# Optimization experiments

Hardware: AMD Instinct MI355X
Metric: run time of the kernel (lower is better)

Reference implementation:

```python
import math
import jax, jax.numpy as jnp
import numpy as np

C, H, R, PD = 256, 6, 32, 16
HEAD_SCALE = 1.0 / math.sqrt(R)


def setup_inputs() -> dict:
    key = jax.random.key(0)
    ks = jax.random.split(key, 8)
    B, Lp1 = 8, 4097
    feats = jax.random.normal(ks[0], (B, Lp1, C), dtype=jnp.float32)
    # params (stored [in, out] for x @ W)
    Wq = jax.random.normal(ks[1], (C, H * R), dtype=jnp.float32) / math.sqrt(C)
    Wk = jax.random.normal(ks[2], (C, H * R), dtype=jnp.float32) / math.sqrt(C)
    Wpi = jax.random.normal(ks[3], (C, PD), dtype=jnp.float32) / math.sqrt(C)
    bpi = jnp.zeros((PD,), jnp.float32)
    Wpj = jax.random.normal(ks[4], (C, PD), dtype=jnp.float32) / math.sqrt(C)
    bpj = jnp.zeros((PD,), jnp.float32)
    Wd = jax.random.normal(ks[5], (C, 1), dtype=jnp.float32) / math.sqrt(C)
    bd = jnp.zeros((1,), jnp.float32)
    alpha_pair = jnp.float32(0.5)
    logit_scale = jnp.float32(1.0)
    return {"feats": feats, "Wq": Wq, "Wk": Wk, "Wpi": Wpi, "bpi": bpi,
            "Wpj": Wpj, "bpj": bpj, "Wd": Wd, "bd": bd,
            "alpha_pair": alpha_pair, "logit_scale": logit_scale}


def _fold_vertices(feats):
    x = feats[:, 1:]                      # drop first token
    B, L, Cc = x.shape
    return x.reshape(B, L // 2, 2, Cc).mean(axis=2)  # [B, N, C]


def reference(feats, Wq, Wk, Wpi, bpi, Wpj, bpj, Wd, bd, alpha_pair, logit_scale):
    x = _fold_vertices(feats)             # [B, N, C]
    B, N, _ = x.shape
    Q = (x @ Wq).reshape(B, N, H, R)
    K = (x @ Wk).reshape(B, N, H, R)
    # sum over heads fused into one contraction (math-equal to per-head scores summed)
    S = jnp.einsum('bnhr,bmhr->bnm', Q, K) * HEAD_SCALE   # [B, N, N]
    a_i = jax.nn.relu(x @ Wpi + bpi)      # [B, N, PD]
    b_j = jax.nn.relu(x @ Wpj + bpj)
    S = S + jnp.maximum(alpha_pair, 0.0) * jnp.einsum('bnd,bmd->bnm', a_i, b_j)
    d = (x @ Wd + bd)[..., 0]             # [B, N]
    idx = jnp.arange(N)
    S = S.at[:, idx, idx].add(d)
    return S * jnp.maximum(logit_scale, 0.01)
```

## Files before the change

### kernel.cpp

```cpp
#include <hip/hip_runtime.h>
#include <hip/hip_bf16.h>
#include <stdint.h>

typedef __attribute__((ext_vector_type(8))) short short8;
typedef __attribute__((ext_vector_type(4))) short short4v;
typedef __attribute__((ext_vector_type(4))) float f32x4;
typedef __attribute__((ext_vector_type(4))) unsigned uint4v;

#define NB 8
#define NN 2048
#define CC 256
#define LP1 4097
#define HR 192
#define PDim 16
#define KP 224
#define NPAD 448
#define HEAD_SCALE 0.17677669529663689f

#define GLOAD16(g, l) __builtin_amdgcn_global_load_lds( \
    (const __attribute__((address_space(1))) unsigned int*)(g), \
    (__attribute__((address_space(3))) unsigned int*)(l), 16, 0, 0)

static __device__ __forceinline__ unsigned short bf16bits(float f) {
    __hip_bfloat16 h = __float2bfloat16(f);
    return *(unsigned short*)&h;
}

__global__ __launch_bounds__(256) void k0_prep(
    const float* __restrict__ Wq, const float* __restrict__ Wk,
    const float* __restrict__ Wpi, const float* __restrict__ Wpj,
    const float* __restrict__ Wd,
    __hip_bfloat16* __restrict__ WT,
    unsigned* __restrict__ Ppad, unsigned* __restrict__ Rpad)
{
    const int WTN = NPAD*CC;
    const int PV  = NB*NN*2;
    int i = blockIdx.x*blockDim.x + threadIdx.x;
    if (i < WTN) {
        int c = i >> 8, k = i & 255;
        float v;
        if (c < HR)                 v = Wq[k*HR + c] * HEAD_SCALE;
        else if (c < 2*HR)          v = Wk[k*HR + (c-HR)];
        else if (c < 2*HR+PDim)     v = Wpi[k*PDim + (c-2*HR)];
        else if (c < 2*HR+2*PDim)   v = Wpj[k*PDim + (c-2*HR-PDim)];
        else if (c == 416)          v = Wd[k];
        else                        v = 0.f;
        WT[i] = __float2bfloat16(v);
    } else {
        int j = i - WTN;
        unsigned* arr = (j < PV) ? Ppad : Rpad;
        int q = (j < PV) ? j : j - PV;
        int row = q >> 1, of = 104 + (q & 1)*4;
        *(uint4v*)(arr + (size_t)row*(KP/2) + of) = (uint4v){0,0,0,0};
    }
}

__global__ __launch_bounds__(256, 3) void ka_proj(
    const float* __restrict__ feats, const __hip_bfloat16* __restrict__ WT,
    const float* __restrict__ bpi, const float* __restrict__ bpj,
    const float* __restrict__ bd, const float* __restrict__ alpha_pair,
    __hip_bfloat16* __restrict__ P, __hip_bfloat16* __restrict__ R,
    float* __restrict__ dvec)
{
    __shared__ __hip_bfloat16 ldsA[32*256];
    __shared__ __hip_bfloat16 ldsB[448*32];

    int t = threadIdx.x;
    int lane = t & 63;
    int w = t >> 6;
    int l15 = lane & 15, lg = lane >> 4;
    int hw = blockIdx.x;
    int b = hw & 7;
    int n0loc = (hw >> 3) * 32;

    int scol = (((t & 3) ^ ((t >> 4) & 3)) << 4);
    const char* srcB[7];
    int wofB[7];
#pragma unroll
    for (int i = 0; i < 7; ++i) {
        int row = i*64 + (t >> 2);
        srcB[i] = (const char*)WT + (size_t)row*512 + scol;
        wofB[i] = row*64 + ((t & 3) << 4);
    }

    uint4v st[7];
#pragma unroll
    for (int i = 0; i < 7; ++i) st[i] = *(const uint4v*)(srcB[i]);

    {
        int r = t >> 3, cg = t & 7;
        size_t fb = ((size_t)b*LP1 + 1 + 2*(size_t)(n0loc + r))*CC + cg*32;
#pragma unroll
        for (int s = 0; s < 4; ++s) {
            float4 a0 = *(const float4*)(feats + fb + s*8);
            float4 a1 = *(const float4*)(feats + fb + s*8 + 4);
            float4 c0 = *(const float4*)(feats + fb + CC + s*8);
            float4 c1 = *(const float4*)(feats + fb + CC + s*8 + 4);
            unsigned short h[8];
            h[0] = bf16bits(0.5f*(a0.x + c0.x));
            h[1] = bf16bits(0.5f*(a0.y + c0.y));
            h[2] = bf16bits(0.5f*(a0.z + c0.z));
            h[3] = bf16bits(0.5f*(a0.w + c0.w));
            h[4] = bf16bits(0.5f*(a1.x + c1.x));
            h[5] = bf16bits(0.5f*(a1.y + c1.y));
            h[6] = bf16bits(0.5f*(a1.z + c1.z));
            h[7] = bf16bits(0.5f*(a1.w + c1.w));
            int slot = (cg*4 + s) ^ (r & 7);
            *(short8*)((char*)ldsA + r*512 + slot*16) = *(const short8*)h;
        }
    }

#pragma unroll
    for (int i = 0; i < 7; ++i)
        *(uint4v*)((char*)ldsB + wofB[i]) = st[i];
    __syncthreads();

    f32x4 acc[7][2];
#pragma unroll
    for (int ni = 0; ni < 7; ++ni)
#pragma unroll
        for (int mi = 0; mi < 2; ++mi)
            acc[ni][mi] = (f32x4){0.f, 0.f, 0.f, 0.f};

    int arow[2];
#pragma unroll
    for (int mi = 0; mi < 2; ++mi) arow[mi] = (mi*16 + l15)*512;
    int rx = l15 & 7;
    int bbase = (w*112 + l15)*64 + ((lg ^ ((l15 >> 2) & 3)) << 4);

#pragma unroll
    for (int kk = 0; kk < 8; ++kk) {
        if (kk < 7) {
#pragma unroll
            for (int i = 0; i < 7; ++i)
                st[i] = *(const uint4v*)(srcB[i] + (size_t)(kk + 1)*64);
        }
        short8 a[2], bb[7];
        int slotb = ((kk*4 + lg) ^ rx) << 4;
#pragma unroll
        for (int mi = 0; mi < 2; ++mi)
            a[mi] = *(const short8*)((const char*)ldsA + arow[mi] + slotb);
#pragma unroll
        for (int ni = 0; ni < 7; ++ni)
            bb[ni] = *(const short8*)((const char*)ldsB + bbase + ni*1024);
#pragma unroll
        for (int ni = 0; ni < 7; ++ni)
#pragma unroll
            for (int mi = 0; mi < 2; ++mi)
                acc[ni][mi] = __builtin_amdgcn_mfma_f32_16x16x32_bf16(
                    bb[ni], a[mi], acc[ni][mi], 0, 0, 0);

        __syncthreads();
        if (kk < 7) {
#pragma unroll
            for (int i = 0; i < 7; ++i)
                *(uint4v*)((char*)ldsB + wofB[i]) = st[i];
            __syncthreads();
        }
    }

    float alpha_eff = fmaxf(alpha_pair[0], 0.f);
    float bd0 = bd[0];
#pragma unroll
    for (int ni = 0; ni < 7; ++ni) {
        int cb = w*112 + ni*16 + lg*4;
#pragma unroll
        for (int mi = 0; mi < 2; ++mi) {
            int n = n0loc + mi*16 + l15;
            size_t rb = ((size_t)b*NN + n)*KP;
            f32x4 v = acc[ni][mi];
            if (cb < HR) {
                short4v h;
#pragma unroll
                for (int j = 0; j < 4; ++j) h[j] = (short)bf16bits(v[j]);
                *(short4v*)(P + rb + cb) = h;
            } else if (cb < 2*HR) {
                short4v h;
#pragma unroll
                for (int j = 0; j < 4; ++j) h[j] = (short)bf16bits(v[j]);
                *(short4v*)(R + rb + (cb - HR)) = h;
            } else if (cb < 2*HR + PDim) {
                int pc = cb - 2*HR;
                short4v h;
#pragma unroll
                for (int j = 0; j < 4; ++j)
                    h[j] = (short)bf16bits(fmaxf(v[j] + bpi[pc+j], 0.f) * alpha_eff);
                *(short4v*)(P + rb + HR + pc) = h;
            } else if (cb < 2*HR + 2*PDim) {
                int pc = cb - 2*HR - PDim;
                short4v h;
#pragma unroll
                for (int j = 0; j < 4; ++j)
                    h[j] = (short)bf16bits(fmaxf(v[j] + bpj[pc+j], 0.f));
                *(short4v*)(R + rb + HR + pc) = h;
            } else if (cb == 416) {
                dvec[(size_t)b*NN + n] = v[0] + bd0;
            }
        }
    }
}

__global__ __launch_bounds__(256, 4) void kb_pair(
    const __hip_bfloat16* __restrict__ P, const __hip_bfloat16* __restrict__ R,
    const float* __restrict__ dvec, const float* __restrict__ logit_scale,
    float* __restrict__ out)
{
    __shared__ __hip_bfloat16 ldsA[2][128*32];
    __shared__ __hip_bfloat16 ldsB[2][128*32];

    int t = threadIdx.x;
    int lane = t & 63;
    int w = t >> 6;
    int wr = w >> 1, wc = w & 1;
    int l15 = lane & 15, lg = lane >> 4;

    int hw = blockIdx.x;
    int b = hw & 7;
    int within = hw >> 3;
    int m0 = (within & 15) << 7;
    int n0 = (within >> 4) << 7;

    const char* srcA[2];
    const char* srcB[2];
    {
        int scolb = (((t & 3) ^ ((t >> 4) & 3)) << 4);
#pragma unroll
        for (int i = 0; i < 2; ++i) {
            int row = i*64 + (t >> 2);
            srcA[i] = (const char*)(P + ((size_t)b*NN + n0 + row)*KP) + scolb;
            srcB[i] = (const char*)(R + ((size_t)b*NN + m0 + row)*KP) + scolb;
        }
    }
    int ldst = w * 1024;

    int abyte = (wr*64 + l15)*64 + ((lg ^ ((l15 >> 2) & 3)) << 4);
    int bbyte = (wc*64 + l15)*64 + ((lg ^ ((l15 >> 2) & 3)) << 4);

    f32x4 acc[4][4];
#pragma unroll
    for (int ni = 0; ni < 4; ++ni)
#pragma unroll
        for (int mi = 0; mi < 4; ++mi)
            acc[ni][mi] = (f32x4){0.f, 0.f, 0.f, 0.f};

#pragma unroll
    for (int i = 0; i < 2; ++i) {
        GLOAD16(srcA[i], (char*)(&ldsA[0][0]) + i*4096 + ldst);
        GLOAD16(srcB[i], (char*)(&ldsB[0][0]) + i*4096 + ldst);
    }
#pragma unroll
    for (int i = 0; i < 2; ++i) {
        GLOAD16(srcA[i] + 64, (char*)(&ldsA[1][0]) + i*4096 + ldst);
        GLOAD16(srcB[i] + 64, (char*)(&ldsB[1][0]) + i*4096 + ldst);
    }

#pragma unroll
    for (int s = 0; s < 7; ++s) {
        if (s < 6) asm volatile("s_waitcnt vmcnt(4)" ::: "memory");
        else       asm volatile("s_waitcnt vmcnt(0)" ::: "memory");
        __builtin_amdgcn_s_barrier();
        __builtin_amdgcn_sched_barrier(0);

        const int buf = s & 1;
        short8 a[4], bb[4];
#pragma unroll
        for (int mi = 0; mi < 4; ++mi)
            a[mi] = *(const short8*)((const char*)(&ldsA[buf][0]) + abyte + mi*1024);
#pragma unroll
        for (int ni = 0; ni < 4; ++ni)
            bb[ni] = *(const short8*)((const char*)(&ldsB[buf][0]) + bbyte + ni*1024);
#pragma unroll
        for (int ni = 0; ni < 4; ++ni)
#pragma unroll
            for (int mi = 0; mi < 4; ++mi)
                acc[ni][mi] = __builtin_amdgcn_mfma_f32_16x16x32_bf16(
                    bb[ni], a[mi], acc[ni][mi], 0, 0, 0);

        __builtin_amdgcn_sched_barrier(0);
        __builtin_amdgcn_s_barrier();
        if (s + 2 < 7) {
            size_t kof = (size_t)(s + 2) * 64;
#pragma unroll
            for (int i = 0; i < 2; ++i) {
                GLOAD16(srcA[i] + kof, (char*)(&ldsA[buf][0]) + i*4096 + ldst);
                GLOAD16(srcB[i] + kof, (char*)(&ldsB[buf][0]) + i*4096 + ldst);
            }
        }
    }

    float ls = fmaxf(logit_scale[0], 0.01f);
    bool diag_tile = (n0 == m0);
#pragma unroll
    for (int mi = 0; mi < 4; ++mi) {
        int orow = n0 + wr*64 + mi*16 + l15;
        float* orow_p = out + ((size_t)b*NN + orow)*NN;
        float dval = diag_tile ? dvec[(size_t)b*NN + orow] : 0.f;
#pragma unroll
        for (int ni = 0; ni < 4; ++ni) {
            int cbase = m0 + wc*64 + ni*16 + lg*4;
            f32x4 v = acc[ni][mi];
            if (diag_tile) {
                int dj = orow - cbase;
                if (dj >= 0 && dj < 4) v[dj] += dval;
            }
            f32x4 o;
#pragma unroll
            for (int j = 0; j < 4; ++j) o[j] = v[j] * ls;
            *(f32x4*)(orow_p + cbase) = o;
        }
    }
}

extern "C" void kernel_launch(void* const* d_in, const int* in_sizes, int n_in,
                              void* d_out, int out_size, void* d_ws, size_t ws_size,
                              hipStream_t stream)
{
    const float* feats = (const float*)d_in[0];
    const float* Wq    = (const float*)d_in[1];
    const float* Wk    = (const float*)d_in[2];
    const float* Wpi   = (const float*)d_in[3];
    const float* bpi   = (const float*)d_in[4];
    const float* Wpj   = (const float*)d_in[5];
    const float* bpj   = (const float*)d_in[6];
    const float* Wd    = (const float*)d_in[7];
    const float* bd    = (const float*)d_in[8];
    const float* alpha = (const float*)d_in[9];
    const float* lsc   = (const float*)d_in[10];

    char* ws = (char*)d_ws;
    __hip_bfloat16* WT = (__hip_bfloat16*)(ws);
    __hip_bfloat16* P  = (__hip_bfloat16*)(ws + 229376);
    __hip_bfloat16* R  = (__hip_bfloat16*)(ws + 7569408);
    float*          dv = (float*)(ws + 14909440);

    k0_prep<<<704, 256, 0, stream>>>(Wq, Wk, Wpi, Wpj, Wd,
                                     WT, (unsigned*)P, (unsigned*)R);
    ka_proj<<<512, 256, 0, stream>>>(feats, WT, bpi, bpj, bd, alpha, P, R, dv);
    kb_pair<<<2048, 256, 0, stream>>>(P, R, dv, lsc, (float*)d_out);
}
```

Baseline: 63.96 us.

## Compute two adjacent column tiles per block with a continuous load pipeline

```diff
diff --git a/kernel.cpp b/kernel.cpp
--- a/kernel.cpp
+++ b/kernel.cpp
@@ -216,9 +216,10 @@
 
     int hw = blockIdx.x;
     int b = hw & 7;
-    int within = hw >> 3;
-    int m0 = (within & 15) << 7;
-    int n0 = (within >> 4) << 7;
+    int p = hw >> 3;
+    int n0 = (p >> 3) << 7;
+    int m0base = (p & 7) << 8;
+    const size_t TOFF = 128 * KP * 2;
 
     const char* srcA[2];
     const char* srcB[2];
@@ -228,7 +229,7 @@
         for (int i = 0; i < 2; ++i) {
             int row = i*64 + (t >> 2);
             srcA[i] = (const char*)(P + ((size_t)b*NN + n0 + row)*KP) + scolb;
-            srcB[i] = (const char*)(R + ((size_t)b*NN + m0 + row)*KP) + scolb;
+            srcB[i] = (const char*)(R + ((size_t)b*NN + m0base + row)*KP) + scolb;
         }
     }
     int ldst = w * 1024;
@@ -236,6 +237,8 @@
     int abyte = (wr*64 + l15)*64 + ((lg ^ ((l15 >> 2) & 3)) << 4);
     int bbyte = (wc*64 + l15)*64 + ((lg ^ ((l15 >> 2) & 3)) << 4);
 
+    float ls = fmaxf(logit_scale[0], 0.01f);
+
     f32x4 acc[4][4];
 #pragma unroll
     for (int ni = 0; ni < 4; ++ni)
@@ -243,24 +246,17 @@
         for (int mi = 0; mi < 4; ++mi)
             acc[ni][mi] = (f32x4){0.f, 0.f, 0.f, 0.f};
 
-#pragma unroll
-    for (int i = 0; i < 2; ++i) {
-        GLOAD16(srcA[i], (char*)(&ldsA[0][0]) + i*4096 + ldst);
-        GLOAD16(srcB[i], (char*)(&ldsB[0][0]) + i*4096 + ldst);
-    }
-#pragma unroll
-    for (int i = 0; i < 2; ++i) {
-        GLOAD16(srcA[i] + 64, (char*)(&ldsA[1][0]) + i*4096 + ldst);
-        GLOAD16(srcB[i] + 64, (char*)(&ldsB[1][0]) + i*4096 + ldst);
-    }
-
-#pragma unroll
-    for (int s = 0; s < 7; ++s) {
-        if (s < 6) asm volatile("s_waitcnt vmcnt(4)" ::: "memory");
-        else       asm volatile("s_waitcnt vmcnt(0)" ::: "memory");
-        __builtin_amdgcn_s_barrier();
-        __builtin_amdgcn_sched_barrier(0);
-
+    auto STAGE = [&](int step) {
+        size_t kof = (size_t)(step % 7) * 64;
+        size_t bof = (step >= 7) ? TOFF : 0;
+        int buf = step & 1;
+        GLOAD16(srcA[0] + kof,       (char*)(&ldsA[buf][0]) + 0*4096 + ldst);
+        GLOAD16(srcB[0] + bof + kof, (char*)(&ldsB[buf][0]) + 0*4096 + ldst);
+        GLOAD16(srcA[1] + kof,       (char*)(&ldsA[buf][0]) + 1*4096 + ldst);
+        GLOAD16(srcB[1] + bof + kof, (char*)(&ldsB[buf][0]) + 1*4096 + ldst);
+    };
+
+    auto COMPUTE = [&](int s) {
         const int buf = s & 1;
         short8 a[4], bb[4];
 #pragma unroll
@@ -275,40 +271,65 @@
             for (int mi = 0; mi < 4; ++mi)
                 acc[ni][mi] = __builtin_amdgcn_mfma_f32_16x16x32_bf16(
                     bb[ni], a[mi], acc[ni][mi], 0, 0, 0);
-
+    };
+
+    auto EPILOGUE = [&](int m0t) {
+        bool diag_tile = (n0 == m0t);
+#pragma unroll
+        for (int mi = 0; mi < 4; ++mi) {
+            int orow = n0 + wr*64 + mi*16 + l15;
+            float* orow_p = out + ((size_t)b*NN + orow)*NN;
+            float dval = diag_tile ? dvec[(size_t)b*NN + orow] : 0.f;
+#pragma unroll
+            for (int ni = 0; ni < 4; ++ni) {
+                int cbase = m0t + wc*64 + ni*16 + lg*4;
+                f32x4 v = acc[ni][mi];
+                if (diag_tile) {
+                    int dj = orow - cbase;
+                    if (dj >= 0 && dj < 4) v[dj] += dval;
+                }
+                f32x4 o;
+#pragma unroll
+                for (int j = 0; j < 4; ++j) o[j] = v[j] * ls;
+                *(f32x4*)(orow_p + cbase) = o;
+            }
+        }
+    };
+
+    STAGE(0);
+    STAGE(1);
+
+#pragma unroll
+    for (int s = 0; s < 7; ++s) {
+        asm volatile("s_waitcnt vmcnt(4)" ::: "memory");
+        __builtin_amdgcn_s_barrier();
+        __builtin_amdgcn_sched_barrier(0);
+        COMPUTE(s);
         __builtin_amdgcn_sched_barrier(0);
         __builtin_amdgcn_s_barrier();
-        if (s + 2 < 7) {
-            size_t kof = (size_t)(s + 2) * 64;
-#pragma unroll
-            for (int i = 0; i < 2; ++i) {
-                GLOAD16(srcA[i] + kof, (char*)(&ldsA[buf][0]) + i*4096 + ldst);
-                GLOAD16(srcB[i] + kof, (char*)(&ldsB[buf][0]) + i*4096 + ldst);
-            }
-        }
-    }
-
-    float ls = fmaxf(logit_scale[0], 0.01f);
-    bool diag_tile = (n0 == m0);
-#pragma unroll
-    for (int mi = 0; mi < 4; ++mi) {
-        int orow = n0 + wr*64 + mi*16 + l15;
-        float* orow_p = out + ((size_t)b*NN + orow)*NN;
-        float dval = diag_tile ? dvec[(size_t)b*NN + orow] : 0.f;
-#pragma unroll
-        for (int ni = 0; ni < 4; ++ni) {
-            int cbase = m0 + wc*64 + ni*16 + lg*4;
-            f32x4 v = acc[ni][mi];
-            if (diag_tile) {
-                int dj = orow - cbase;
-                if (dj >= 0 && dj < 4) v[dj] += dval;
-            }
-            f32x4 o;
-#pragma unroll
-            for (int j = 0; j < 4; ++j) o[j] = v[j] * ls;
-            *(f32x4*)(orow_p + cbase) = o;
-        }
-    }
+        STAGE(s + 2);
+    }
+
+    EPILOGUE(m0base);
+#pragma unroll
+    for (int ni = 0; ni < 4; ++ni)
+#pragma unroll
+        for (int mi = 0; mi < 4; ++mi)
+            acc[ni][mi] = (f32x4){0.f, 0.f, 0.f, 0.f};
+
+#pragma unroll
+    for (int s = 7; s < 14; ++s) {
+        if (s < 13) asm volatile("s_waitcnt vmcnt(4)" ::: "memory");
+        else        asm volatile("s_waitcnt vmcnt(0)" ::: "memory");
+        __builtin_amdgcn_s_barrier();
+        __builtin_amdgcn_sched_barrier(0);
+        COMPUTE(s);
+        __builtin_amdgcn_sched_barrier(0);
+        __builtin_amdgcn_s_barrier();
+        if (s + 2 < 14) STAGE(s + 2);
+    }
+
+    EPILOGUE(m0base + 128);
 }
 
 extern "C" void kernel_launch(void* const* d_in, const int* in_sizes, int n_in,
@@ -336,5 +357,5 @@
     k0_prep<<<704, 256, 0, stream>>>(Wq, Wk, Wpi, Wpj, Wd,
                                      WT, (unsigned*)P, (unsigned*)R);
     ka_proj<<<512, 256, 0, stream>>>(feats, WT, bpi, bpj, bd, alpha, P, R, dv);
-    kb_pair<<<2048, 256, 0, stream>>>(P, R, dv, lsc, (float*)d_out);
-}
+    kb_pair<<<1024, 256, 0, stream>>>(P, R, dv, lsc, (float*)d_out);
+}
```

Measured after the change: 76.17 us. 19.1% more time.
